# Performance work log

Hardware: AMD Instinct MI355X
Metric: run time of the kernel (lower is better)

Reference implementation:

```python
import jax, jax.numpy as jnp
import numpy as np

CHEB_K = 3


def _cheb(support):
    # Chebyshev polynomial basis [I, A, 2A@T_{k-1} - T_{k-2}] of a dense (N,N) support
    N = support.shape[0]
    ks = [jnp.eye(N, dtype=support.dtype), support]
    for _ in range(2, CHEB_K):
        ks.append(2.0 * support @ ks[-1] - ks[-2])
    return ks


def _agcn(x, sk, W, b):
    # x: (B,N,C); sk: list of (N,N); W: (2*cheb_k*C, O)
    xg = jnp.concatenate([jnp.einsum('nm,bmc->bnc', s, x) for s in sk], axis=-1)
    return jnp.einsum('bni,io->bno', xg, W) + b


def _cell(x, h, sk, Wg, bg, Wu, bu):
    # adaptive graph-conv GRU cell
    hd = h.shape[-1]
    zr = jax.nn.sigmoid(_agcn(jnp.concatenate([x, h], axis=-1), sk, Wg, bg))
    z, r = zr[..., :hd], zr[..., hd:]
    hc = jnp.tanh(_agcn(jnp.concatenate([x, z * h], axis=-1), sk, Wu, bu))
    return r * h + (1.0 - r) * hc


def _forward(x, targets_time, Memory, Wq, We1, We2, egW, egb, euW, eub, dgW, dgb, duW, dub, pW, pb):
    x = jnp.swapaxes(x, 1, -1)  # (B,L,N,C)
    B, L, N, C = x.shape
    H = targets_time.shape[-1]
    ycov = jnp.swapaxes(targets_time, 1, -1)           # (B,H,1,ycov_dim)
    ycov = jnp.broadcast_to(ycov, (B, H, N, ycov.shape[-1]))
    # adaptive adjacency from memory
    e1 = We1 @ Memory
    e2 = We2 @ Memory
    g1 = jax.nn.softmax(jax.nn.relu(e1 @ e2.T), axis=-1)
    g2 = jax.nn.softmax(jax.nn.relu(e2 @ e1.T), axis=-1)
    sk = _cheb(g1) + _cheb(g2)                         # 2*cheb_k supports
    rnn_units = egb.shape[0] // 2
    h0 = jnp.zeros((B, N, rnn_units), x.dtype)
    # encoder: unroll over L (num_layers = 1)
    def enc_step(h, xt):
        return _cell(xt, h, sk, egW, egb, euW, eub), None
    h_t, _ = jax.lax.scan(enc_step, h0, jnp.swapaxes(x, 0, 1))
    # memory attention
    query = h_t @ Wq                                    # (B,N,mem_dim)
    att = jax.nn.softmax(query @ Memory.T, axis=-1)     # (B,N,mem_num)
    h_att = att @ Memory
    h_de = jnp.concatenate([h_t, h_att], axis=-1)       # (B,N,rnn+mem)
    out_dim = pb.shape[0]
    go0 = jnp.zeros((B, N, out_dim), x.dtype)
    def dec_step(carry, yc):
        go, h = carry
        h = _cell(jnp.concatenate([go, yc], axis=-1), h, sk, dgW, dgb, duW, dub)
        go = h @ pW + pb
        return (go, h), go
    _, outs = jax.lax.scan(dec_step, (go0, h_de), jnp.swapaxes(ycov, 0, 1))
    out = jnp.swapaxes(outs, 0, 1)                      # (B,H,N,out_dim)
    return jnp.swapaxes(out, 1, -1)                     # (B,out_dim,N,H)


def setup_inputs() -> dict:
    key = jax.random.key(0)
    ks = jax.random.split(key, 20)
    B, N, L, H = 64, 512, 12, 12
    in_dim, out_dim, ycov_dim = 1, 1, 5
    rnn, mem_num, mem_dim = 64, 20, 64
    dec_dim = rnn + mem_dim
    s = 0.1
    inp = {
        'x': jax.random.normal(ks[0], (B, in_dim, N, L), jnp.float32),
        'adj': jax.random.uniform(ks[1], (N, N), jnp.float32),
        'targets': jax.random.normal(ks[2], (B, out_dim, N, H), jnp.float32),
        'targets_time': jax.random.normal(ks[3], (B, ycov_dim, 1, H), jnp.float32),
        'index': 100,
        'Memory': jax.random.normal(ks[4], (mem_num, mem_dim), jnp.float32) * s,
        'Wq': jax.random.normal(ks[5], (rnn, mem_dim), jnp.float32) * s,
        'We1': jax.random.normal(ks[6], (N, mem_num), jnp.float32) * s,
        'We2': jax.random.normal(ks[7], (N, mem_num), jnp.float32) * s,
        'enc_gate_W': jax.random.normal(ks[8], (2 * CHEB_K * (in_dim + rnn), 2 * rnn), jnp.float32) * s,
        'enc_gate_b': jnp.zeros((2 * rnn,), jnp.float32),
        'enc_upd_W': jax.random.normal(ks[9], (2 * CHEB_K * (in_dim + rnn), rnn), jnp.float32) * s,
        'enc_upd_b': jnp.zeros((rnn,), jnp.float32),
        'dec_gate_W': jax.random.normal(ks[10], (2 * CHEB_K * (out_dim + ycov_dim + dec_dim), 2 * dec_dim), jnp.float32) * s,
        'dec_gate_b': jnp.zeros((2 * dec_dim,), jnp.float32),
        'dec_upd_W': jax.random.normal(ks[11], (2 * CHEB_K * (out_dim + ycov_dim + dec_dim), dec_dim), jnp.float32) * s,
        'dec_upd_b': jnp.zeros((dec_dim,), jnp.float32),
        'proj_W': jax.random.normal(ks[12], (dec_dim, out_dim), jnp.float32) * s,
        'proj_b': jnp.zeros((out_dim,), jnp.float32),
    }
    return inp


def reference(x, adj, targets, targets_time, index, Memory, Wq, We1, We2, enc_gate_W, enc_gate_b, enc_upd_W, enc_upd_b, dec_gate_W, dec_gate_b, dec_upd_W, dec_upd_b, proj_W, proj_b):
    # adj, targets, index only used in training mode; eval path ignores them
    return _forward(x, targets_time, Memory, Wq, We1, We2, enc_gate_W, enc_gate_b, enc_upd_W, enc_upd_b, dec_gate_W, dec_gate_b, dec_upd_W, dec_upd_b, proj_W, proj_b)
```

## Files before the change

### kernel.cpp

```cpp
#include <hip/hip_runtime.h>
#include <hip/hip_bf16.h>
#include <math.h>

typedef __hip_bfloat16 bf16;
typedef __attribute__((ext_vector_type(8))) short s8v;
typedef __attribute__((ext_vector_type(4))) short s4v;
typedef __attribute__((ext_vector_type(4))) float f4v;

#define B_   64
#define N_   512
#define L_   12
#define H_   12
#define RNN  64
#define MEMN 20
#define MEMD 64
#define DD   128
#define NB   32768


__device__ inline void glds16(const bf16* g, bf16* l) {
  __builtin_amdgcn_global_load_lds((const __attribute__((address_space(1))) void*)g,
                                   (__attribute__((address_space(3))) void*)l, 16, 0, 0);
}

__device__ inline int2 xcd_swz() {
  int lid = blockIdx.x + blockIdx.y * gridDim.x;
  int chunk = (gridDim.x * gridDim.y) >> 3;
  int swz = (lid & 7) * chunk + (lid >> 3);
  int bx = swz / gridDim.y;
  int by = swz - bx * gridDim.y;
  return make_int2(bx, by);
}

template<int C_CH, int CP>
__global__ __launch_bounds__(256) void gemm_mix(
    const bf16* __restrict__ Sb, const bf16* __restrict__ XT, bf16* __restrict__ Yb) {
  const int NCOLS = 64 * C_CH;
  __shared__ bf16 As[128 * 32];
  __shared__ bf16 Bs[128 * 32];
  const int tid = threadIdx.x, lane = tid & 63, wid = tid >> 6;
  const int wr = wid >> 1, wc = wid & 1;
  int2 sz = xcd_swz();
  const int bn = sz.x * 128, bm = sz.y * 128;
  const int r_in = lane >> 2, dslot = lane & 3;
  f4v acc[4][4] = {};
  for (int k0 = 0; k0 < 512; k0 += 32) {
#pragma unroll
    for (int h = 0; h < 2; h++) {
      int ci = wid + h * 4;
      int row = ci * 16 + r_in;
      int ss = dslot ^ ((row >> 1) & 3);
      glds16(Sb + (size_t)(bm + row) * 512 + k0 + ss * 8, As + ci * 512);
      glds16(XT + (size_t)(bn + row) * 512 + k0 + ss * 8, Bs + ci * 512);
    }
    asm volatile("s_waitcnt vmcnt(0)" ::: "memory");
    __syncthreads();
    s8v a[4], bb[4];
#pragma unroll
    for (int m = 0; m < 4; m++) {
      int row = wr * 64 + m * 16 + (lane & 15);
      int slot = (lane >> 4) ^ ((row >> 1) & 3);
      a[m] = *(const s8v*)(As + row * 32 + slot * 8);
    }
#pragma unroll
    for (int n = 0; n < 4; n++) {
      int col = wc * 64 + n * 16 + (lane & 15);
      int slot = (lane >> 4) ^ ((col >> 1) & 3);
      bb[n] = *(const s8v*)(Bs + col * 32 + slot * 8);
    }
#pragma unroll
    for (int m = 0; m < 4; m++)
#pragma unroll
      for (int n = 0; n < 4; n++)
        acc[m][n] = __builtin_amdgcn_mfma_f32_16x16x32_bf16(a[m], bb[n], acc[m][n], 0, 0, 0);
    __syncthreads();
  }
#pragma unroll
  for (int m = 0; m < 4; m++) {
#pragma unroll
    for (int rg = 0; rg < 4; rg++) {
      int row = bm + wr * 64 + m * 16 + (lane >> 4) * 4 + rg;
      int s = row >> 9, nn = row & 511;
      size_t obase = (size_t)s * NB * CP;
#pragma unroll
      for (int n = 0; n < 4; n++) {
        int col = bn + wc * 64 + n * 16 + (lane & 15);
        if (col < NCOLS) {
          int b2 = col / C_CH, c = col - b2 * C_CH;
          Yb[obase + (size_t)(b2 * 512 + nn) * CP + c] = __float2bfloat16(acc[m][n][rg]);
        }
      }
    }
  }
}

template<int CP, int EPI, int CCH>
__global__ __launch_bounds__(256) void gemm_proj(
    const bf16* __restrict__ WT, const bf16* __restrict__ XCin,
    const bf16* __restrict__ Yb, const float* __restrict__ bias,
    bf16* __restrict__ RG, float* __restrict__ HT, int hd,
    const float* __restrict__ pW, const float* __restrict__ pb,
    float* __restrict__ outp, bf16* __restrict__ XTo, bf16* __restrict__ XCo,
    bf16* __restrict__ XTa, bf16* __restrict__ XCa, int t) {
  __shared__ bf16 As[128 * 32];
  __shared__ bf16 Bs[64 * 32];
  __shared__ float red2[8 * 64];
  __shared__ float pws[128];
  const int tid = threadIdx.x, lane = tid & 63, wid = tid >> 6;
  const int wr = wid >> 1, wc = wid & 1;
  int2 sz = xcd_swz();
  const int r0 = sz.x * 64, bm = sz.y * 128;
  const int Opad = gridDim.y * 128;
  const int r_in = lane >> 2, dslot = lane & 3;

  if (EPI == 2 && tid < 128) pws[tid] = pW[tid];

  f4v acc[4][2] = {};
#pragma unroll
  for (int seg = 0; seg < 5; seg++) {
    const bf16* Bbase = (seg == 0) ? XCin : (Yb + (size_t)(seg - 1) * NB * CP);
    const bf16* Abase = WT + (size_t)seg * Opad * CP;
    for (int k0 = 0; k0 < CP; k0 += 32) {
#pragma unroll
      for (int h = 0; h < 2; h++) {
        int ci = wid + h * 4;
        int row = ci * 16 + r_in;
        int ss = dslot ^ ((row >> 1) & 3);
        glds16(Abase + (size_t)(bm + row) * CP + k0 + ss * 8, As + ci * 512);
      }
      {
        int row = wid * 16 + r_in;
        int ss = dslot ^ ((row >> 1) & 3);
        glds16(Bbase + (size_t)(r0 + row) * CP + k0 + ss * 8, Bs + wid * 512);
      }
      asm volatile("s_waitcnt vmcnt(0)" ::: "memory");
      __syncthreads();
      s8v a[4], bb[2];
#pragma unroll
      for (int m = 0; m < 4; m++) {
        int row = wr * 64 + m * 16 + (lane & 15);
        int slot = (lane >> 4) ^ ((row >> 1) & 3);
        a[m] = *(const s8v*)(As + row * 32 + slot * 8);
      }
#pragma unroll
      for (int n = 0; n < 2; n++) {
        int col = wc * 32 + n * 16 + (lane & 15);
        int slot = (lane >> 4) ^ ((col >> 1) & 3);
        bb[n] = *(const s8v*)(Bs + col * 32 + slot * 8);
      }
#pragma unroll
      for (int m = 0; m < 4; m++)
#pragma unroll
        for (int n = 0; n < 2; n++)
          acc[m][n] = __builtin_amdgcn_mfma_f32_16x16x32_bf16(a[m], bb[n], acc[m][n], 0, 0, 0);
      __syncthreads();
    }
  }

#pragma unroll
  for (int m = 0; m < 4; m++) {
#pragma unroll
    for (int n = 0; n < 2; n++) {
      int r = r0 + wc * 32 + n * 16 + (lane & 15);
      int b = r >> 9, nn = r & 511;
      int ch0 = bm + wr * 64 + m * 16 + (lane >> 4) * 4;
      if (EPI == 0) {
        if (ch0 < hd) {
          bf16 z4[4];
#pragma unroll
          for (int rg = 0; rg < 4; rg++) {
            int o = ch0 + rg;
            float sg = 1.f / (1.f + expf(-(acc[m][n][rg] + bias[o])));
            float hold = HT[(size_t)o * NB + r];
            z4[rg] = __float2bfloat16(sg * hold);
            XTo[((size_t)b * CCH + o) * 512 + nn] = z4[rg];
          }
          *(s4v*)(XCo + (size_t)r * CP + ch0) = *(const s4v*)z4;
        } else {
#pragma unroll
          for (int rg = 0; rg < 4; rg++) {
            int o = ch0 + rg;
            float sg = 1.f / (1.f + expf(-(acc[m][n][rg] + bias[o])));
            RG[(size_t)(o - hd) * NB + r] = __float2bfloat16(sg);
          }
        }
      } else {
        if (ch0 < hd) {
          bf16 h4[4];
#pragma unroll
          for (int rg = 0; rg < 4; rg++) {
            int o = ch0 + rg;
            float hc = tanhf(acc[m][n][rg] + bias[o]);
            float rgt = __bfloat162float(RG[(size_t)o * NB + r]);
            float* hp = HT + (size_t)o * NB + r;
            float hn = rgt * (*hp) + (1.f - rgt) * hc;
            *hp = hn;
            h4[rg] = __float2bfloat16(hn);
            XTo[((size_t)b * CCH + o) * 512 + nn] = h4[rg];
            acc[m][n][rg] = hn;
          }
          *(s4v*)(XCo + (size_t)r * CP + ch0) = *(const s4v*)h4;
        }
      }
    }
  }

  if (EPI == 2) {
    int slot = wr * 4 + (lane >> 4);
#pragma unroll
    for (int n = 0; n < 2; n++) {
      int r_local = wc * 32 + n * 16 + (lane & 15);
      float ps = 0.f;
#pragma unroll
      for (int m = 0; m < 4; m++)
#pragma unroll
        for (int rg = 0; rg < 4; rg++) {
          int o = wr * 64 + m * 16 + (lane >> 4) * 4 + rg;
          ps += acc[m][n][rg] * pws[o];
        }
      red2[slot * 64 + r_local] = ps;
    }
    __syncthreads();
    if (tid < 64) {
      float v = pb[0];
#pragma unroll
      for (int s2 = 0; s2 < 8; s2++) v += red2[s2 * 64 + tid];
      int r = r0 + tid;
      int b = r >> 9, nn = r & 511;
      outp[b * 6144 + nn * 12 + t] = v;
      bf16 gb = __float2bfloat16(v);
      XTo[((size_t)b * CCH + hd) * 512 + nn] = gb;
      XCo[(size_t)r * CP + hd] = gb;
      XTa[((size_t)b * CCH + hd) * 512 + nn] = gb;
      XCa[(size_t)r * CP + hd] = gb;
    }
  }
}

__global__ __launch_bounds__(256) void gemm_cheb(
    const bf16* __restrict__ A, const bf16* __restrict__ BT, bf16* __restrict__ O) {
  __shared__ bf16 As[128 * 32];
  __shared__ bf16 Bs[128 * 32];
  const int tid = threadIdx.x, lane = tid & 63, wid = tid >> 6;
  const int wr = wid >> 1, wc = wid & 1;
  const int bm = blockIdx.y * 128, bn = blockIdx.x * 128;
  const int r_in = lane >> 2, dslot = lane & 3;
  f4v acc[4][4] = {};
  for (int k0 = 0; k0 < 512; k0 += 32) {
#pragma unroll
    for (int h = 0; h < 2; h++) {
      int ci = wid + h * 4;
      int row = ci * 16 + r_in;
      int ss = dslot ^ ((row >> 1) & 3);
      glds16(A + (size_t)(bm + row) * 512 + k0 + ss * 8, As + ci * 512);
      glds16(BT + (size_t)(bn + row) * 512 + k0 + ss * 8, Bs + ci * 512);
    }
    asm volatile("s_waitcnt vmcnt(0)" ::: "memory");
    __syncthreads();
    s8v a[4], bb[4];
#pragma unroll
    for (int m = 0; m < 4; m++) {
      int row = wr * 64 + m * 16 + (lane & 15);
      int slot = (lane >> 4) ^ ((row >> 1) & 3);
      a[m] = *(const s8v*)(As + row * 32 + slot * 8);
    }
#pragma unroll
    for (int n = 0; n < 4; n++) {
      int col = wc * 64 + n * 16 + (lane & 15);
      int slot = (lane >> 4) ^ ((col >> 1) & 3);
      bb[n] = *(const s8v*)(Bs + col * 32 + slot * 8);
    }
#pragma unroll
    for (int m = 0; m < 4; m++)
#pragma unroll
      for (int n = 0; n < 4; n++)
        acc[m][n] = __builtin_amdgcn_mfma_f32_16x16x32_bf16(a[m], bb[n], acc[m][n], 0, 0, 0);
    __syncthreads();
  }
#pragma unroll
  for (int m = 0; m < 4; m++) {
#pragma unroll
    for (int rg = 0; rg < 4; rg++) {
      int row = bm + wr * 64 + m * 16 + (lane >> 4) * 4 + rg;
#pragma unroll
      for (int n = 0; n < 4; n++) {
        int col = bn + wc * 64 + n * 16 + (lane & 15);
        float v = 2.f * acc[m][n][rg] - (row == col ? 1.f : 0.f);
        O[(size_t)row * 512 + col] = __float2bfloat16(v);
      }
    }
  }
}

__global__ void fill_zero4(float4* p, int n) {
  for (int i = blockIdx.x * 256 + threadIdx.x; i < n; i += gridDim.x * 256)
    p[i] = make_float4(0.f, 0.f, 0.f, 0.f);
}

__global__ void compute_e(const float* __restrict__ We1, const float* __restrict__ We2,
                          const float* __restrict__ Mem, float* __restrict__ e1,
                          float* __restrict__ e2) {
  int idx = blockIdx.x * 256 + threadIdx.x;
  if (idx >= N_ * MEMD) return;
  int n = idx >> 6, d = idx & 63;
  float s1 = 0.f, s2 = 0.f;
  for (int k = 0; k < MEMN; k++) {
    float m = Mem[k * MEMD + d];
    s1 += We1[n * MEMN + k] * m;
    s2 += We2[n * MEMN + k] * m;
  }
  e1[idx] = s1; e2[idx] = s2;
}

__global__ void compute_wqm(const float* __restrict__ Wq, const float* __restrict__ Mem,
                            float* __restrict__ WqM) {
  int idx = blockIdx.x * 256 + threadIdx.x;
  if (idx >= RNN * MEMN) return;
  int c = idx / MEMN, j = idx - c * MEMN;
  float s = 0.f;
  for (int d = 0; d < MEMD; d++) s += Wq[c * MEMD + d] * Mem[j * MEMD + d];
  WqM[idx] = s;
}

__global__ void scores_relu(const float* __restrict__ e1, const float* __restrict__ e2,
                            float* __restrict__ S) {
  int idx = blockIdx.x * 256 + threadIdx.x;
  if (idx >= N_ * N_) return;
  int n = idx >> 9, m = idx & 511;
  float s = 0.f;
  for (int k = 0; k < MEMD; k++) s += e1[n * MEMD + k] * e2[m * MEMD + k];
  S[idx] = s > 0.f ? s : 0.f;
}

__global__ __launch_bounds__(256)
void row_softmax(const float* __restrict__ S, float* __restrict__ G) {
  int r = blockIdx.x;
  __shared__ float red[256];
  float m = -1e30f;
  for (int j = threadIdx.x; j < N_; j += 256) m = fmaxf(m, S[r * N_ + j]);
  red[threadIdx.x] = m; __syncthreads();
  for (int s = 128; s > 0; s >>= 1) {
    if (threadIdx.x < s) red[threadIdx.x] = fmaxf(red[threadIdx.x], red[threadIdx.x + s]);
    __syncthreads();
  }
  m = red[0]; __syncthreads();
  float sum = 0.f;
  for (int j = threadIdx.x; j < N_; j += 256) sum += expf(S[r * N_ + j] - m);
  red[threadIdx.x] = sum; __syncthreads();
  for (int s = 128; s > 0; s >>= 1) {
    if (threadIdx.x < s) red[threadIdx.x] += red[threadIdx.x + s];
    __syncthreads();
  }
  float inv = 1.f / red[0];
  for (int j = threadIdx.x; j < N_; j += 256)
    G[r * N_ + j] = expf(S[r * N_ + j] - m) * inv;
}

__global__ void trans_f32(const float* __restrict__ in, float* __restrict__ outT) {
  __shared__ float t[32][33];
  int bx = blockIdx.x * 32, by = blockIdx.y * 32;
  int x = threadIdx.x, y = threadIdx.y;
  for (int i = 0; i < 32; i += 8) t[y + i][x] = in[(by + y + i) * 512 + bx + x];
  __syncthreads();
  for (int i = 0; i < 32; i += 8) outT[(bx + y + i) * 512 + by + x] = t[x][y + i];
}

__global__ void trans_to_bf16(const float* __restrict__ in, bf16* __restrict__ outN,
                              bf16* __restrict__ outT) {
  __shared__ float t[32][33];
  int bx = blockIdx.x * 32, by = blockIdx.y * 32;
  int x = threadIdx.x, y = threadIdx.y;
  for (int i = 0; i < 32; i += 8) {
    float v = in[(by + y + i) * 512 + bx + x];
    t[y + i][x] = v;
    outN[(by + y + i) * 512 + bx + x] = __float2bfloat16(v);
  }
  __syncthreads();
  for (int i = 0; i < 32; i += 8)
    outT[(bx + y + i) * 512 + by + x] = __float2bfloat16(t[x][y + i]);
}

__global__ void prep_wt(const float* __restrict__ W, bf16* __restrict__ WT,
                        int C, int O, int Opad, int CP, int HD, int MC) {
  int idx = blockIdx.x * 256 + threadIdx.x;
  int tot = 5 * Opad * CP;
  if (idx >= tot) return;
  int seg = idx / (Opad * CP);
  int rem = idx - seg * (Opad * CP);
  int o = rem / CP, c = rem - (rem / CP) * CP;
  float v = 0.f;
  int srcc = -1;
  if (c < HD) srcc = MC + c;
  else if (c < HD + MC) srcc = c - HD;
  if (srcc >= 0 && o < O) {
    const int blkmap[5] = {0, 1, 2, 4, 5};
    int blk = blkmap[seg];
    v = W[(blk * C + srcc) * O + o];
    if (seg == 0) v += W[(3 * C + srcc) * O + o];
  }
  WT[idx] = __float2bfloat16(v);
}

__global__ void fill_misc_enc(bf16* __restrict__ XTh, bf16* __restrict__ XTz,
                              bf16* __restrict__ XCh, bf16* __restrict__ XCz,
                              const float* __restrict__ x, int t) {
  int r = blockIdx.x * 256 + threadIdx.x;
  if (r >= NB) return;
  int b = r >> 9, n = r & 511;
  bf16 v = __float2bfloat16(x[b * 6144 + n * 12 + t]);
  XTh[((size_t)b * 65 + 64) * 512 + n] = v;
  XTz[((size_t)b * 65 + 64) * 512 + n] = v;
  XCh[(size_t)r * 96 + 64] = v;
  XCz[(size_t)r * 96 + 64] = v;
}

__global__ void fill_misc_dec(bf16* __restrict__ XTh, bf16* __restrict__ XTz,
                              bf16* __restrict__ XCh, bf16* __restrict__ XCz,
                              const float* __restrict__ tt, int t, int writego) {
  int idx = blockIdx.x * 256 + threadIdx.x;
  if (idx >= NB * 6) return;
  int ch = idx >> 15, r = idx & (NB - 1);
  int b = r >> 9, n = r & 511;
  bf16 v;
  int c;
  if (ch < 5) { v = __float2bfloat16(tt[b * 60 + ch * 12 + t]); c = 129 + ch; }
  else { if (!writego) return; v = __float2bfloat16(0.f); c = 128; }
  XTh[((size_t)b * 134 + c) * 512 + n] = v;
  XTz[((size_t)b * 134 + c) * 512 + n] = v;
  XCh[(size_t)r * 160 + c] = v;
  XCz[(size_t)r * 160 + c] = v;
}

__global__ __launch_bounds__(128) void attention2(
    const float* __restrict__ HbT, const float* __restrict__ WqM,
    const float* __restrict__ Mem, float* __restrict__ HdT,
    bf16* __restrict__ XTh, bf16* __restrict__ XCh) {
  __shared__ float h[64][128];
  __shared__ float wqm[64][20];
  __shared__ float mem[20][64];
  const int tid = threadIdx.x, r0 = blockIdx.x * 128;
  const int r = r0 + tid, b = r >> 9, n = r & 511;
  for (int e = tid; e < 64 * 128; e += 128) {
    int c = e >> 7, j = e & 127;
    h[c][j] = HbT[(size_t)c * NB + r0 + j];
  }
  for (int e = tid; e < 1280; e += 128) {
    wqm[e / 20][e % 20] = WqM[e];
    mem[e >> 6][e & 63] = Mem[e];
  }
  __syncthreads();
  float s[20];
#pragma unroll
  for (int j = 0; j < 20; j++) s[j] = 0.f;
  for (int c = 0; c < 64; c++) {
    float hv = h[c][tid];
#pragma unroll
    for (int j = 0; j < 20; j++) s[j] += hv * wqm[c][j];
  }
  float mx = s[0];
#pragma unroll
  for (int j = 1; j < 20; j++) mx = fmaxf(mx, s[j]);
  float sum = 0.f;
#pragma unroll
  for (int j = 0; j < 20; j++) { s[j] = expf(s[j] - mx); sum += s[j]; }
  float inv = 1.f / sum;
#pragma unroll
  for (int j = 0; j < 20; j++) s[j] *= inv;
  for (int d = 0; d < 64; d++) {
    float ha = 0.f;
#pragma unroll
    for (int j = 0; j < 20; j++) ha += s[j] * mem[j][d];
    float hv = h[d][tid];
    HdT[(size_t)d * NB + r] = hv;
    HdT[(size_t)(64 + d) * NB + r] = ha;
    bf16 hb = __float2bfloat16(hv), ab = __float2bfloat16(ha);
    XTh[((size_t)b * 134 + d) * 512 + n] = hb;
    XTh[((size_t)b * 134 + 64 + d) * 512 + n] = ab;
    XCh[(size_t)r * 160 + d] = hb;
    XCh[(size_t)r * 160 + 64 + d] = ab;
  }
}

extern "C" void kernel_launch(void* const* d_in, const int* in_sizes, int n_in,
                              void* d_out, int out_size, void* d_ws, size_t ws_size,
                              hipStream_t stream) {
  const float* x   = (const float*)d_in[0];
  const float* tt  = (const float*)d_in[3];
  const float* Mem = (const float*)d_in[5];
  const float* Wq  = (const float*)d_in[6];
  const float* We1 = (const float*)d_in[7];
  const float* We2 = (const float*)d_in[8];
  const float* egW = (const float*)d_in[9];
  const float* egb = (const float*)d_in[10];
  const float* euW = (const float*)d_in[11];
  const float* eub = (const float*)d_in[12];
  const float* dgW = (const float*)d_in[13];
  const float* dgb = (const float*)d_in[14];
  const float* duW = (const float*)d_in[15];
  const float* dub = (const float*)d_in[16];
  const float* pW  = (const float*)d_in[17];
  const float* pb  = (const float*)d_in[18];
  float* out = (float*)d_out;

  char* ws = (char*)d_ws;
  size_t off = 0;
  auto alloc = [&](size_t bytes) { char* p = ws + off; off += (bytes + 255) & ~(size_t)255; return p; };
  bf16* XTh   = (bf16*)alloc((size_t)8576 * 512 * 2);
  bf16* XCh   = (bf16*)alloc((size_t)NB * 160 * 2);
  float* HbT  = (float*)alloc((size_t)RNN * NB * 4);
  size_t zero_bytes = off;
  bf16* XTz   = (bf16*)alloc((size_t)8576 * 512 * 2);
  bf16* XCz   = (bf16*)alloc((size_t)NB * 160 * 2);
  bf16* Ybuf  = (bf16*)alloc((size_t)4 * NB * 160 * 2);
  bf16* RG    = (bf16*)alloc((size_t)DD * NB * 2);
  bf16* WTeg  = (bf16*)alloc((size_t)5 * 128 * 96 * 2);
  bf16* WTeu  = (bf16*)alloc((size_t)5 * 128 * 96 * 2);
  bf16* WTdg  = (bf16*)alloc((size_t)5 * 256 * 160 * 2);
  bf16* WTdu  = (bf16*)alloc((size_t)5 * 128 * 160 * 2);
  bf16* Sb    = (bf16*)alloc((size_t)4 * 512 * 512 * 2);
  bf16* g1T   = (bf16*)alloc((size_t)512 * 512 * 2);
  bf16* g2T   = (bf16*)alloc((size_t)512 * 512 * 2);
  float* HdT  = (float*)alloc((size_t)DD * NB * 4);
  float* WqM  = (float*)alloc((size_t)RNN * MEMN * 4);
  float* e1   = (float*)alloc((size_t)N_ * MEMD * 4);
  float* e2   = (float*)alloc((size_t)N_ * MEMD * 4);
  float* S    = (float*)alloc((size_t)N_ * N_ * 4);
  float* ST   = (float*)alloc((size_t)N_ * N_ * 4);
  float* g1f  = (float*)alloc((size_t)N_ * N_ * 4);
  float* g2f  = (float*)alloc((size_t)N_ * N_ * 4);

  auto blk = [](long n) { return dim3((unsigned)((n + 255) / 256)); };

  fill_zero4<<<2048, 256, 0, stream>>>((float4*)ws, (int)(zero_bytes / 16));
  compute_e<<<blk(N_ * MEMD), 256, 0, stream>>>(We1, We2, Mem, e1, e2);
  compute_wqm<<<blk(RNN * MEMN), 256, 0, stream>>>(Wq, Mem, WqM);
  scores_relu<<<blk(N_ * N_), 256, 0, stream>>>(e1, e2, S);
  trans_f32<<<dim3(16, 16), dim3(32, 8), 0, stream>>>(S, ST);
  row_softmax<<<N_, 256, 0, stream>>>(S, g1f);
  row_softmax<<<N_, 256, 0, stream>>>(ST, g2f);
  trans_to_bf16<<<dim3(16, 16), dim3(32, 8), 0, stream>>>(g1f, Sb + 0 * 262144, g1T);
  trans_to_bf16<<<dim3(16, 16), dim3(32, 8), 0, stream>>>(g2f, Sb + 2 * 262144, g2T);
  gemm_cheb<<<dim3(4, 4), 256, 0, stream>>>(Sb + 0 * 262144, g1T, Sb + 1 * 262144);
  gemm_cheb<<<dim3(4, 4), 256, 0, stream>>>(Sb + 2 * 262144, g2T, Sb + 3 * 262144);
  prep_wt<<<blk(5 * 128 * 96), 256, 0, stream>>>(egW, WTeg, 65, 128, 128, 96, 64, 1);
  prep_wt<<<blk(5 * 128 * 96), 256, 0, stream>>>(euW, WTeu, 65, 64, 128, 96, 64, 1);
  prep_wt<<<blk(5 * 256 * 160), 256, 0, stream>>>(dgW, WTdg, 134, 256, 256, 160, 128, 6);
  prep_wt<<<blk(5 * 128 * 160), 256, 0, stream>>>(duW, WTdu, 134, 128, 128, 160, 128, 6);

  for (int t = 0; t < L_; t++) {
    fill_misc_enc<<<blk(NB), 256, 0, stream>>>(XTh, XTz, XCh, XCz, x, t);
    gemm_mix<65, 96><<<dim3(33, 16), 256, 0, stream>>>(Sb, XTh, Ybuf);
    gemm_proj<96, 0, 65><<<dim3(512, 1), 256, 0, stream>>>(
        WTeg, XCh, Ybuf, egb, RG, HbT, RNN, nullptr, nullptr, nullptr,
        XTz, XCz, nullptr, nullptr, 0);
    gemm_mix<65, 96><<<dim3(33, 16), 256, 0, stream>>>(Sb, XTz, Ybuf);
    gemm_proj<96, 1, 65><<<dim3(512, 1), 256, 0, stream>>>(
        WTeu, XCz, Ybuf, eub, RG, HbT, RNN, nullptr, nullptr, nullptr,
        XTh, XCh, nullptr, nullptr, 0);
  }

  attention2<<<dim3(256), 128, 0, stream>>>(HbT, WqM, Mem, HdT, XTh, XCh);

  for (int t = 0; t < H_; t++) {
    fill_misc_dec<<<blk((long)NB * 6), 256, 0, stream>>>(XTh, XTz, XCh, XCz, tt, t, t == 0);
    gemm_mix<134, 160><<<dim3(67, 16), 256, 0, stream>>>(Sb, XTh, Ybuf);
    gemm_proj<160, 0, 134><<<dim3(512, 2), 256, 0, stream>>>(
        WTdg, XCh, Ybuf, dgb, RG, HdT, DD, nullptr, nullptr, nullptr,
        XTz, XCz, nullptr, nullptr, 0);
    gemm_mix<134, 160><<<dim3(67, 16), 256, 0, stream>>>(Sb, XTz, Ybuf);
    gemm_proj<160, 2, 134><<<dim3(512, 1), 256, 0, stream>>>(
        WTdu, XCz, Ybuf, dub, RG, HdT, DD, pW, pb, out,
        XTh, XCh, XTz, XCz, t);
  }
}
```

Measured before the change: 2.620 ms.

## Fuse graph-mixing GEMM and weight projection into one GRU kernel per gate

Replaces the separate support-mixing GEMM (S@X written to a global Ybuf) and the projection GEMM with a single kernel. Each 512-thread block owns 64 rows and computes the four support products for them, keeping the mixed result in LDS and projecting it straight through the weights. This removes the large intermediate global round-trip and halves the launches per step. The cost is that each block recomputes S-tile loads per 64-row block, the weight fragments are read directly from global memory with no staging, and the inner GEMMs are small with a barrier on every k-step.

```diff
diff --git a/kernel.cpp b/kernel.cpp
--- a/kernel.cpp
+++ b/kernel.cpp
@@ -23,164 +23,151 @@
                                    (__attribute__((address_space(3))) void*)l, 16, 0, 0);
 }
 
-__device__ inline int2 xcd_swz() {
-  int lid = blockIdx.x + blockIdx.y * gridDim.x;
-  int chunk = (gridDim.x * gridDim.y) >> 3;
-  int swz = (lid & 7) * chunk + (lid >> 3);
-  int bx = swz / gridDim.y;
-  int by = swz - bx * gridDim.y;
-  return make_int2(bx, by);
-}
-
-template<int C_CH, int CP>
-__global__ __launch_bounds__(256) void gemm_mix(
-    const bf16* __restrict__ Sb, const bf16* __restrict__ XT, bf16* __restrict__ Yb) {
-  const int NCOLS = 64 * C_CH;
-  __shared__ bf16 As[128 * 32];
-  __shared__ bf16 Bs[128 * 32];
-  const int tid = threadIdx.x, lane = tid & 63, wid = tid >> 6;
-  const int wr = wid >> 1, wc = wid & 1;
-  int2 sz = xcd_swz();
-  const int bn = sz.x * 128, bm = sz.y * 128;
-  const int r_in = lane >> 2, dslot = lane & 3;
-  f4v acc[4][4] = {};
-  for (int k0 = 0; k0 < 512; k0 += 32) {
-#pragma unroll
-    for (int h = 0; h < 2; h++) {
-      int ci = wid + h * 4;
-      int row = ci * 16 + r_in;
-      int ss = dslot ^ ((row >> 1) & 3);
-      glds16(Sb + (size_t)(bm + row) * 512 + k0 + ss * 8, As + ci * 512);
-      glds16(XT + (size_t)(bn + row) * 512 + k0 + ss * 8, Bs + ci * 512);
-    }
-    asm volatile("s_waitcnt vmcnt(0)" ::: "memory");
-    __syncthreads();
-    s8v a[4], bb[4];
-#pragma unroll
-    for (int m = 0; m < 4; m++) {
-      int row = wr * 64 + m * 16 + (lane & 15);
-      int slot = (lane >> 4) ^ ((row >> 1) & 3);
-      a[m] = *(const s8v*)(As + row * 32 + slot * 8);
-    }
-#pragma unroll
-    for (int n = 0; n < 4; n++) {
-      int col = wc * 64 + n * 16 + (lane & 15);
-      int slot = (lane >> 4) ^ ((col >> 1) & 3);
-      bb[n] = *(const s8v*)(Bs + col * 32 + slot * 8);
-    }
-#pragma unroll
-    for (int m = 0; m < 4; m++)
-#pragma unroll
-      for (int n = 0; n < 4; n++)
-        acc[m][n] = __builtin_amdgcn_mfma_f32_16x16x32_bf16(a[m], bb[n], acc[m][n], 0, 0, 0);
-    __syncthreads();
-  }
-#pragma unroll
-  for (int m = 0; m < 4; m++) {
-#pragma unroll
-    for (int rg = 0; rg < 4; rg++) {
-      int row = bm + wr * 64 + m * 16 + (lane >> 4) * 4 + rg;
-      int s = row >> 9, nn = row & 511;
-      size_t obase = (size_t)s * NB * CP;
-#pragma unroll
-      for (int n = 0; n < 4; n++) {
-        int col = bn + wc * 64 + n * 16 + (lane & 15);
-        if (col < NCOLS) {
-          int b2 = col / C_CH, c = col - b2 * C_CH;
-          Yb[obase + (size_t)(b2 * 512 + nn) * CP + c] = __float2bfloat16(acc[m][n][rg]);
-        }
-      }
-    }
-  }
-}
-
-template<int CP, int EPI, int CCH>
-__global__ __launch_bounds__(256) void gemm_proj(
-    const bf16* __restrict__ WT, const bf16* __restrict__ XCin,
-    const bf16* __restrict__ Yb, const float* __restrict__ bias,
-    bf16* __restrict__ RG, float* __restrict__ HT, int hd,
+__device__ inline s8v fragld(const bf16* __restrict__ P, int R0, int ld, int k0, int lane) {
+  return *(const s8v*)(P + (size_t)(R0 + (lane & 15)) * ld + k0 + (lane >> 4) * 8);
+}
+
+template<int C_CH, int CP, int OPAD, int EPI>
+__global__ __launch_bounds__(512) void gru_fused(
+    const bf16* __restrict__ Sb, const bf16* __restrict__ XTin,
+    const bf16* __restrict__ XCin, const bf16* __restrict__ WT,
+    const float* __restrict__ bias, bf16* __restrict__ RG,
+    float* __restrict__ HT, int hd,
     const float* __restrict__ pW, const float* __restrict__ pb,
     float* __restrict__ outp, bf16* __restrict__ XTo, bf16* __restrict__ XCo,
     bf16* __restrict__ XTa, bf16* __restrict__ XCa, int t) {
-  __shared__ bf16 As[128 * 32];
-  __shared__ bf16 Bs[64 * 32];
-  __shared__ float red2[8 * 64];
+  constexpr int YLD = CP + 8;
+  constexpr int MPW = OPAD / 4;
+  constexpr int MF  = MPW / 16;
+  constexpr int CF  = CP / 32;
+  constexpr int NCH = 4 + CP / 16;
+  __shared__ bf16 A1[64 * 32];
+  __shared__ bf16 B1[CP * 32];
+  __shared__ bf16 BsX[64 * 32];
+  __shared__ bf16 Ylds[64 * YLD];
+  __shared__ float red2[16 * 64];
   __shared__ float pws[128];
   const int tid = threadIdx.x, lane = tid & 63, wid = tid >> 6;
-  const int wr = wid >> 1, wc = wid & 1;
-  int2 sz = xcd_swz();
-  const int r0 = sz.x * 64, bm = sz.y * 128;
-  const int Opad = gridDim.y * 128;
+  const int wo = wid >> 1, wn = wid & 1;
+  const int wr1 = wid >> 1, wc1 = wid & 1;
+  int swb = (blockIdx.x & 7) * (gridDim.x >> 3) + (blockIdx.x >> 3);
+  const int r0 = swb * 64;
+  const int b = r0 >> 9, n0 = r0 & 511;
   const int r_in = lane >> 2, dslot = lane & 3;
 
   if (EPI == 2 && tid < 128) pws[tid] = pW[tid];
 
-  f4v acc[4][2] = {};
-#pragma unroll
-  for (int seg = 0; seg < 5; seg++) {
-    const bf16* Bbase = (seg == 0) ? XCin : (Yb + (size_t)(seg - 1) * NB * CP);
-    const bf16* Abase = WT + (size_t)seg * Opad * CP;
-    for (int k0 = 0; k0 < CP; k0 += 32) {
-#pragma unroll
-      for (int h = 0; h < 2; h++) {
-        int ci = wid + h * 4;
-        int row = ci * 16 + r_in;
-        int ss = dslot ^ ((row >> 1) & 3);
-        glds16(Abase + (size_t)(bm + row) * CP + k0 + ss * 8, As + ci * 512);
-      }
-      {
-        int row = wid * 16 + r_in;
-        int ss = dslot ^ ((row >> 1) & 3);
-        glds16(Bbase + (size_t)(r0 + row) * CP + k0 + ss * 8, Bs + wid * 512);
+  f4v acc2[MF][2] = {};
+
+  for (int k0 = 0; k0 < CP; k0 += 32) {
+    if (wid < 4) {
+      int row = wid * 16 + r_in;
+      int ss = dslot ^ ((row >> 1) & 3);
+      glds16(XCin + (size_t)(r0 + row) * CP + k0 + ss * 8, BsX + wid * 512);
+    }
+    asm volatile("s_waitcnt vmcnt(0)" ::: "memory");
+    __syncthreads();
+    s8v a[MF], bb[2];
+#pragma unroll
+    for (int m = 0; m < MF; m++) a[m] = fragld(WT, wo * MPW + m * 16, CP, k0, lane);
+#pragma unroll
+    for (int n = 0; n < 2; n++) {
+      int rl = wn * 32 + n * 16 + (lane & 15);
+      int slot = (lane >> 4) ^ ((rl >> 1) & 3);
+      bb[n] = *(const s8v*)(BsX + rl * 32 + slot * 8);
+    }
+#pragma unroll
+    for (int m = 0; m < MF; m++)
+#pragma unroll
+      for (int n = 0; n < 2; n++)
+        acc2[m][n] = __builtin_amdgcn_mfma_f32_16x16x32_bf16(a[m], bb[n], acc2[m][n], 0, 0, 0);
+    __syncthreads();
+  }
+
+  for (int s = 0; s < 4; s++) {
+    f4v acc1[CF] = {};
+    const bf16* Sbase = Sb + (size_t)s * 512 * 512;
+    for (int k0 = 0; k0 < 512; k0 += 32) {
+      for (int ci = wid; ci < NCH; ci += 8) {
+        if (ci < 4) {
+          int row = ci * 16 + r_in;
+          int ss = dslot ^ ((row >> 1) & 3);
+          glds16(Sbase + (size_t)(n0 + row) * 512 + k0 + ss * 8, A1 + ci * 512);
+        } else {
+          int crow = (ci - 4) * 16 + r_in;
+          int ss = dslot ^ ((crow >> 1) & 3);
+          glds16(XTin + ((size_t)b * C_CH + crow) * 512 + k0 + ss * 8, B1 + (ci - 4) * 512);
+        }
       }
       asm volatile("s_waitcnt vmcnt(0)" ::: "memory");
       __syncthreads();
-      s8v a[4], bb[2];
-#pragma unroll
-      for (int m = 0; m < 4; m++) {
-        int row = wr * 64 + m * 16 + (lane & 15);
+      s8v a1;
+      {
+        int row = wr1 * 16 + (lane & 15);
         int slot = (lane >> 4) ^ ((row >> 1) & 3);
-        a[m] = *(const s8v*)(As + row * 32 + slot * 8);
-      }
+        a1 = *(const s8v*)(A1 + row * 32 + slot * 8);
+      }
+#pragma unroll
+      for (int f = 0; f < CF; f++) {
+        int col = wc1 * (CP / 2) + f * 16 + (lane & 15);
+        int slot = (lane >> 4) ^ ((col >> 1) & 3);
+        s8v b1 = *(const s8v*)(B1 + col * 32 + slot * 8);
+        acc1[f] = __builtin_amdgcn_mfma_f32_16x16x32_bf16(a1, b1, acc1[f], 0, 0, 0);
+      }
+      __syncthreads();
+    }
+#pragma unroll
+    for (int f = 0; f < CF; f++)
+#pragma unroll
+      for (int rg = 0; rg < 4; rg++) {
+        int row = wr1 * 16 + (lane >> 4) * 4 + rg;
+        int col = wc1 * (CP / 2) + f * 16 + (lane & 15);
+        Ylds[row * YLD + col] = __float2bfloat16(acc1[f][rg]);
+      }
+    __syncthreads();
+    const bf16* Ab = WT + (size_t)(s + 1) * OPAD * CP;
+#pragma unroll
+    for (int k0 = 0; k0 < CP; k0 += 32) {
+      s8v a[MF], bb[2];
+#pragma unroll
+      for (int m = 0; m < MF; m++) a[m] = fragld(Ab, wo * MPW + m * 16, CP, k0, lane);
 #pragma unroll
       for (int n = 0; n < 2; n++) {
-        int col = wc * 32 + n * 16 + (lane & 15);
-        int slot = (lane >> 4) ^ ((col >> 1) & 3);
-        bb[n] = *(const s8v*)(Bs + col * 32 + slot * 8);
-      }
-#pragma unroll
-      for (int m = 0; m < 4; m++)
+        int rl = wn * 32 + n * 16 + (lane & 15);
+        bb[n] = *(const s8v*)(Ylds + rl * YLD + k0 + (lane >> 4) * 8);
+      }
+#pragma unroll
+      for (int m = 0; m < MF; m++)
 #pragma unroll
         for (int n = 0; n < 2; n++)
-          acc[m][n] = __builtin_amdgcn_mfma_f32_16x16x32_bf16(a[m], bb[n], acc[m][n], 0, 0, 0);
-      __syncthreads();
-    }
-  }
-
-#pragma unroll
-  for (int m = 0; m < 4; m++) {
+          acc2[m][n] = __builtin_amdgcn_mfma_f32_16x16x32_bf16(a[m], bb[n], acc2[m][n], 0, 0, 0);
+    }
+  }
+
+#pragma unroll
+  for (int m = 0; m < MF; m++) {
 #pragma unroll
     for (int n = 0; n < 2; n++) {
-      int r = r0 + wc * 32 + n * 16 + (lane & 15);
-      int b = r >> 9, nn = r & 511;
-      int ch0 = bm + wr * 64 + m * 16 + (lane >> 4) * 4;
+      int r = r0 + wn * 32 + n * 16 + (lane & 15);
+      int b2 = r >> 9, nn = r & 511;
+      int ch0 = wo * MPW + m * 16 + (lane >> 4) * 4;
       if (EPI == 0) {
         if (ch0 < hd) {
           bf16 z4[4];
 #pragma unroll
           for (int rg = 0; rg < 4; rg++) {
             int o = ch0 + rg;
-            float sg = 1.f / (1.f + expf(-(acc[m][n][rg] + bias[o])));
+            float sg = 1.f / (1.f + expf(-(acc2[m][n][rg] + bias[o])));
             float hold = HT[(size_t)o * NB + r];
             z4[rg] = __float2bfloat16(sg * hold);
-            XTo[((size_t)b * CCH + o) * 512 + nn] = z4[rg];
+            XTo[((size_t)b2 * C_CH + o) * 512 + nn] = z4[rg];
           }
           *(s4v*)(XCo + (size_t)r * CP + ch0) = *(const s4v*)z4;
         } else {
 #pragma unroll
           for (int rg = 0; rg < 4; rg++) {
             int o = ch0 + rg;
-            float sg = 1.f / (1.f + expf(-(acc[m][n][rg] + bias[o])));
+            float sg = 1.f / (1.f + expf(-(acc2[m][n][rg] + bias[o])));
             RG[(size_t)(o - hd) * NB + r] = __float2bfloat16(sg);
           }
         }
@@ -190,14 +177,14 @@
 #pragma unroll
           for (int rg = 0; rg < 4; rg++) {
             int o = ch0 + rg;
-            float hc = tanhf(acc[m][n][rg] + bias[o]);
+            float hc = tanhf(acc2[m][n][rg] + bias[o]);
             float rgt = __bfloat162float(RG[(size_t)o * NB + r]);
             float* hp = HT + (size_t)o * NB + r;
             float hn = rgt * (*hp) + (1.f - rgt) * hc;
             *hp = hn;
             h4[rg] = __float2bfloat16(hn);
-            XTo[((size_t)b * CCH + o) * 512 + nn] = h4[rg];
-            acc[m][n][rg] = hn;
+            XTo[((size_t)b2 * C_CH + o) * 512 + nn] = h4[rg];
+            acc2[m][n][rg] = hn;
           }
           *(s4v*)(XCo + (size_t)r * CP + ch0) = *(const s4v*)h4;
         }
@@ -206,32 +193,32 @@
   }
 
   if (EPI == 2) {
-    int slot = wr * 4 + (lane >> 4);
+    __syncthreads();
 #pragma unroll
     for (int n = 0; n < 2; n++) {
-      int r_local = wc * 32 + n * 16 + (lane & 15);
+      int r_local = wn * 32 + n * 16 + (lane & 15);
       float ps = 0.f;
 #pragma unroll
-      for (int m = 0; m < 4; m++)
+      for (int m = 0; m < MF; m++)
 #pragma unroll
         for (int rg = 0; rg < 4; rg++) {
-          int o = wr * 64 + m * 16 + (lane >> 4) * 4 + rg;
-          ps += acc[m][n][rg] * pws[o];
+          int o = wo * MPW + m * 16 + (lane >> 4) * 4 + rg;
+          ps += acc2[m][n][rg] * pws[o];
         }
-      red2[slot * 64 + r_local] = ps;
+      red2[(wo * 4 + (lane >> 4)) * 64 + r_local] = ps;
     }
     __syncthreads();
     if (tid < 64) {
       float v = pb[0];
 #pragma unroll
-      for (int s2 = 0; s2 < 8; s2++) v += red2[s2 * 64 + tid];
+      for (int s2 = 0; s2 < 16; s2++) v += red2[s2 * 64 + tid];
       int r = r0 + tid;
-      int b = r >> 9, nn = r & 511;
-      outp[b * 6144 + nn * 12 + t] = v;
+      int b2 = r >> 9, nn = r & 511;
+      outp[b2 * 6144 + nn * 12 + t] = v;
       bf16 gb = __float2bfloat16(v);
-      XTo[((size_t)b * CCH + hd) * 512 + nn] = gb;
+      XTo[((size_t)b2 * C_CH + hd) * 512 + nn] = gb;
       XCo[(size_t)r * CP + hd] = gb;
-      XTa[((size_t)b * CCH + hd) * 512 + nn] = gb;
+      XTa[((size_t)b2 * C_CH + hd) * 512 + nn] = gb;
       XCa[(size_t)r * CP + hd] = gb;
     }
   }
@@ -505,16 +492,15 @@
   char* ws = (char*)d_ws;
   size_t off = 0;
   auto alloc = [&](size_t bytes) { char* p = ws + off; off += (bytes + 255) & ~(size_t)255; return p; };
-  bf16* XTh   = (bf16*)alloc((size_t)8576 * 512 * 2);
+  bf16* XTh   = (bf16*)alloc((size_t)8640 * 512 * 2);
   bf16* XCh   = (bf16*)alloc((size_t)NB * 160 * 2);
   float* HbT  = (float*)alloc((size_t)RNN * NB * 4);
   size_t zero_bytes = off;
-  bf16* XTz   = (bf16*)alloc((size_t)8576 * 512 * 2);
+  bf16* XTz   = (bf16*)alloc((size_t)8640 * 512 * 2);
   bf16* XCz   = (bf16*)alloc((size_t)NB * 160 * 2);
-  bf16* Ybuf  = (bf16*)alloc((size_t)4 * NB * 160 * 2);
   bf16* RG    = (bf16*)alloc((size_t)DD * NB * 2);
   bf16* WTeg  = (bf16*)alloc((size_t)5 * 128 * 96 * 2);
-  bf16* WTeu  = (bf16*)alloc((size_t)5 * 128 * 96 * 2);
+  bf16* WTeu  = (bf16*)alloc((size_t)5 * 64 * 96 * 2);
   bf16* WTdg  = (bf16*)alloc((size_t)5 * 256 * 160 * 2);
   bf16* WTdu  = (bf16*)alloc((size_t)5 * 128 * 160 * 2);
   bf16* Sb    = (bf16*)alloc((size_t)4 * 512 * 512 * 2);
@@ -543,19 +529,17 @@
   gemm_cheb<<<dim3(4, 4), 256, 0, stream>>>(Sb + 0 * 262144, g1T, Sb + 1 * 262144);
   gemm_cheb<<<dim3(4, 4), 256, 0, stream>>>(Sb + 2 * 262144, g2T, Sb + 3 * 262144);
   prep_wt<<<blk(5 * 128 * 96), 256, 0, stream>>>(egW, WTeg, 65, 128, 128, 96, 64, 1);
-  prep_wt<<<blk(5 * 128 * 96), 256, 0, stream>>>(euW, WTeu, 65, 64, 128, 96, 64, 1);
+  prep_wt<<<blk(5 * 64 * 96), 256, 0, stream>>>(euW, WTeu, 65, 64, 64, 96, 64, 1);
   prep_wt<<<blk(5 * 256 * 160), 256, 0, stream>>>(dgW, WTdg, 134, 256, 256, 160, 128, 6);
   prep_wt<<<blk(5 * 128 * 160), 256, 0, stream>>>(duW, WTdu, 134, 128, 128, 160, 128, 6);
 
   for (int t = 0; t < L_; t++) {
     fill_misc_enc<<<blk(NB), 256, 0, stream>>>(XTh, XTz, XCh, XCz, x, t);
-    gemm_mix<65, 96><<<dim3(33, 16), 256, 0, stream>>>(Sb, XTh, Ybuf);
-    gemm_proj<96, 0, 65><<<dim3(512, 1), 256, 0, stream>>>(
-        WTeg, XCh, Ybuf, egb, RG, HbT, RNN, nullptr, nullptr, nullptr,
+    gru_fused<65, 96, 128, 0><<<512, 512, 0, stream>>>(
+        Sb, XTh, XCh, WTeg, egb, RG, HbT, RNN, nullptr, nullptr, nullptr,
         XTz, XCz, nullptr, nullptr, 0);
-    gemm_mix<65, 96><<<dim3(33, 16), 256, 0, stream>>>(Sb, XTz, Ybuf);
-    gemm_proj<96, 1, 65><<<dim3(512, 1), 256, 0, stream>>>(
-        WTeu, XCz, Ybuf, eub, RG, HbT, RNN, nullptr, nullptr, nullptr,
+    gru_fused<65, 96, 64, 1><<<512, 512, 0, stream>>>(
+        Sb, XTz, XCz, WTeu, eub, RG, HbT, RNN, nullptr, nullptr, nullptr,
         XTh, XCh, nullptr, nullptr, 0);
   }
 
@@ -563,13 +547,11 @@
 
   for (int t = 0; t < H_; t++) {
     fill_misc_dec<<<blk((long)NB * 6), 256, 0, stream>>>(XTh, XTz, XCh, XCz, tt, t, t == 0);
-    gemm_mix<134, 160><<<dim3(67, 16), 256, 0, stream>>>(Sb, XTh, Ybuf);
-    gemm_proj<160, 0, 134><<<dim3(512, 2), 256, 0, stream>>>(
-        WTdg, XCh, Ybuf, dgb, RG, HdT, DD, nullptr, nullptr, nullptr,
+    gru_fused<134, 160, 256, 0><<<512, 512, 0, stream>>>(
+        Sb, XTh, XCh, WTdg, dgb, RG, HdT, DD, nullptr, nullptr, nullptr,
         XTz, XCz, nullptr, nullptr, 0);
-    gemm_mix<134, 160><<<dim3(67, 16), 256, 0, stream>>>(Sb, XTz, Ybuf);
-    gemm_proj<160, 2, 134><<<dim3(512, 1), 256, 0, stream>>>(
-        WTdu, XCz, Ybuf, dub, RG, HdT, DD, pW, pb, out,
+    gru_fused<134, 160, 128, 2><<<512, 512, 0, stream>>>(
+        Sb, XTz, XCz, WTdu, dub, RG, HdT, DD, pW, pb, out,
         XTh, XCh, XTz, XCz, t);
   }
 }
```

Measured after the change: 2.978 ms. +13.6%, slower.

## Make gemm_proj tile span full output width per block, sized by OPAD template

Applied to the files above, without the earlier changes.

gemm_proj now takes the padded output width as a template parameter, and each block computes all output channels for 64 rows. Each of the four waves owns an OPAD/4 slice of channels across all 64 rows. This removes the second grid row in the decoder gate projection, so the shared activation tiles are loaded once instead of twice. It also stops the encoder update from computing 64 wasted padded channels, since its weights shrink to 64 rows. The cost is larger accumulator and LDS footprints at OPAD=256, which may lower occupancy.

```diff
diff --git a/kernel.cpp b/kernel.cpp
--- a/kernel.cpp
+++ b/kernel.cpp
@@ -94,7 +94,7 @@
   }
 }
 
-template<int CP, int EPI, int CCH>
+template<int CP, int OPAD, int EPI, int CCH>
 __global__ __launch_bounds__(256) void gemm_proj(
     const bf16* __restrict__ WT, const bf16* __restrict__ XCin,
     const bf16* __restrict__ Yb, const float* __restrict__ bias,
@@ -102,68 +102,66 @@
     const float* __restrict__ pW, const float* __restrict__ pb,
     float* __restrict__ outp, bf16* __restrict__ XTo, bf16* __restrict__ XCo,
     bf16* __restrict__ XTa, bf16* __restrict__ XCa, int t) {
-  __shared__ bf16 As[128 * 32];
+  constexpr int MPW = OPAD / 4;
+  constexpr int MF  = MPW / 16;
+  __shared__ bf16 As[OPAD * 32];
   __shared__ bf16 Bs[64 * 32];
-  __shared__ float red2[8 * 64];
+  __shared__ float red2[16 * 64];
   __shared__ float pws[128];
-  const int tid = threadIdx.x, lane = tid & 63, wid = tid >> 6;
-  const int wr = wid >> 1, wc = wid & 1;
-  int2 sz = xcd_swz();
-  const int r0 = sz.x * 64, bm = sz.y * 128;
-  const int Opad = gridDim.y * 128;
+  const int tid = threadIdx.x, lane = tid & 63, wo = tid >> 6;
+  int swb = (blockIdx.x & 7) * (gridDim.x >> 3) + (blockIdx.x >> 3);
+  const int r0 = swb * 64;
   const int r_in = lane >> 2, dslot = lane & 3;
 
   if (EPI == 2 && tid < 128) pws[tid] = pW[tid];
 
-  f4v acc[4][2] = {};
+  f4v acc[MF][4] = {};
 #pragma unroll
   for (int seg = 0; seg < 5; seg++) {
     const bf16* Bbase = (seg == 0) ? XCin : (Yb + (size_t)(seg - 1) * NB * CP);
-    const bf16* Abase = WT + (size_t)seg * Opad * CP;
+    const bf16* Abase = WT + (size_t)seg * OPAD * CP;
     for (int k0 = 0; k0 < CP; k0 += 32) {
-#pragma unroll
-      for (int h = 0; h < 2; h++) {
-        int ci = wid + h * 4;
+      for (int ci = wo; ci < OPAD / 16; ci += 4) {
         int row = ci * 16 + r_in;
         int ss = dslot ^ ((row >> 1) & 3);
-        glds16(Abase + (size_t)(bm + row) * CP + k0 + ss * 8, As + ci * 512);
+        glds16(Abase + (size_t)row * CP + k0 + ss * 8, As + ci * 512);
       }
       {
-        int row = wid * 16 + r_in;
+        int row = wo * 16 + r_in;
         int ss = dslot ^ ((row >> 1) & 3);
-        glds16(Bbase + (size_t)(r0 + row) * CP + k0 + ss * 8, Bs + wid * 512);
+        glds16(Bbase + (size_t)(r0 + row) * CP + k0 + ss * 8, Bs + wo * 512);
       }
       asm volatile("s_waitcnt vmcnt(0)" ::: "memory");
       __syncthreads();
-      s8v a[4], bb[2];
-#pragma unroll
-      for (int m = 0; m < 4; m++) {
-        int row = wr * 64 + m * 16 + (lane & 15);
+      s8v a[MF], bb[4];
+#pragma unroll
+      for (int m = 0; m < MF; m++) {
+        int row = wo * MPW + m * 16 + (lane & 15);
         int slot = (lane >> 4) ^ ((row >> 1) & 3);
         a[m] = *(const s8v*)(As + row * 32 + slot * 8);
       }
 #pragma unroll
-      for (int n = 0; n < 2; n++) {
-        int col = wc * 32 + n * 16 + (lane & 15);
+      for (int n = 0; n < 4; n++) {
+        int col = n * 16 + (lane & 15);
         int slot = (lane >> 4) ^ ((col >> 1) & 3);
         bb[n] = *(const s8v*)(Bs + col * 32 + slot * 8);
       }
 #pragma unroll
-      for (int m = 0; m < 4; m++)
-#pragma unroll
-        for (int n = 0; n < 2; n++)
+      for (int m = 0; m < MF; m++)
+#pragma unroll
+        for (int n = 0; n < 4; n++)
           acc[m][n] = __builtin_amdgcn_mfma_f32_16x16x32_bf16(a[m], bb[n], acc[m][n], 0, 0, 0);
       __syncthreads();
     }
   }
 
 #pragma unroll
-  for (int m = 0; m < 4; m++) {
-#pragma unroll
-    for (int n = 0; n < 2; n++) {
-      int r = r0 + wc * 32 + n * 16 + (lane & 15);
-      int b = r >> 9, nn = r & 511;
-      int ch0 = bm + wr * 64 + m * 16 + (lane >> 4) * 4;
+  for (int m = 0; m < MF; m++) {
+#pragma unroll
+    for (int n = 0; n < 4; n++) {
+      int r = r0 + n * 16 + (lane & 15);
+      int b2 = r >> 9, nn = r & 511;
+      int ch0 = wo * MPW + m * 16 + (lane >> 4) * 4;
       if (EPI == 0) {
         if (ch0 < hd) {
           bf16 z4[4];
@@ -173,7 +171,7 @@
             float sg = 1.f / (1.f + expf(-(acc[m][n][rg] + bias[o])));
             float hold = HT[(size_t)o * NB + r];
             z4[rg] = __float2bfloat16(sg * hold);
-            XTo[((size_t)b * CCH + o) * 512 + nn] = z4[rg];
+            XTo[((size_t)b2 * CCH + o) * 512 + nn] = z4[rg];
           }
           *(s4v*)(XCo + (size_t)r * CP + ch0) = *(const s4v*)z4;
         } else {
@@ -196,7 +194,7 @@
             float hn = rgt * (*hp) + (1.f - rgt) * hc;
             *hp = hn;
             h4[rg] = __float2bfloat16(hn);
-            XTo[((size_t)b * CCH + o) * 512 + nn] = h4[rg];
+            XTo[((size_t)b2 * CCH + o) * 512 + nn] = h4[rg];
             acc[m][n][rg] = hn;
           }
           *(s4v*)(XCo + (size_t)r * CP + ch0) = *(const s4v*)h4;
@@ -206,32 +204,32 @@
   }
 
   if (EPI == 2) {
-    int slot = wr * 4 + (lane >> 4);
-#pragma unroll
-    for (int n = 0; n < 2; n++) {
-      int r_local = wc * 32 + n * 16 + (lane & 15);
+    __syncthreads();
+#pragma unroll
+    for (int n = 0; n < 4; n++) {
+      int r_local = n * 16 + (lane & 15);
       float ps = 0.f;
 #pragma unroll
-      for (int m = 0; m < 4; m++)
+      for (int m = 0; m < MF; m++)
 #pragma unroll
         for (int rg = 0; rg < 4; rg++) {
-          int o = wr * 64 + m * 16 + (lane >> 4) * 4 + rg;
+          int o = wo * MPW + m * 16 + (lane >> 4) * 4 + rg;
           ps += acc[m][n][rg] * pws[o];
         }
-      red2[slot * 64 + r_local] = ps;
+      red2[(wo * 4 + (lane >> 4)) * 64 + r_local] = ps;
     }
     __syncthreads();
     if (tid < 64) {
       float v = pb[0];
 #pragma unroll
-      for (int s2 = 0; s2 < 8; s2++) v += red2[s2 * 64 + tid];
+      for (int s2 = 0; s2 < 16; s2++) v += red2[s2 * 64 + tid];
       int r = r0 + tid;
-      int b = r >> 9, nn = r & 511;
-      outp[b * 6144 + nn * 12 + t] = v;
+      int b2 = r >> 9, nn = r & 511;
+      outp[b2 * 6144 + nn * 12 + t] = v;
       bf16 gb = __float2bfloat16(v);
-      XTo[((size_t)b * CCH + hd) * 512 + nn] = gb;
+      XTo[((size_t)b2 * CCH + hd) * 512 + nn] = gb;
       XCo[(size_t)r * CP + hd] = gb;
-      XTa[((size_t)b * CCH + hd) * 512 + nn] = gb;
+      XTa[((size_t)b2 * CCH + hd) * 512 + nn] = gb;
       XCa[(size_t)r * CP + hd] = gb;
     }
   }
@@ -514,7 +512,7 @@
   bf16* Ybuf  = (bf16*)alloc((size_t)4 * NB * 160 * 2);
   bf16* RG    = (bf16*)alloc((size_t)DD * NB * 2);
   bf16* WTeg  = (bf16*)alloc((size_t)5 * 128 * 96 * 2);
-  bf16* WTeu  = (bf16*)alloc((size_t)5 * 128 * 96 * 2);
+  bf16* WTeu  = (bf16*)alloc((size_t)5 * 64 * 96 * 2);
   bf16* WTdg  = (bf16*)alloc((size_t)5 * 256 * 160 * 2);
   bf16* WTdu  = (bf16*)alloc((size_t)5 * 128 * 160 * 2);
   bf16* Sb    = (bf16*)alloc((size_t)4 * 512 * 512 * 2);
@@ -543,18 +541,18 @@
   gemm_cheb<<<dim3(4, 4), 256, 0, stream>>>(Sb + 0 * 262144, g1T, Sb + 1 * 262144);
   gemm_cheb<<<dim3(4, 4), 256, 0, stream>>>(Sb + 2 * 262144, g2T, Sb + 3 * 262144);
   prep_wt<<<blk(5 * 128 * 96), 256, 0, stream>>>(egW, WTeg, 65, 128, 128, 96, 64, 1);
-  prep_wt<<<blk(5 * 128 * 96), 256, 0, stream>>>(euW, WTeu, 65, 64, 128, 96, 64, 1);
+  prep_wt<<<blk(5 * 64 * 96), 256, 0, stream>>>(euW, WTeu, 65, 64, 64, 96, 64, 1);
   prep_wt<<<blk(5 * 256 * 160), 256, 0, stream>>>(dgW, WTdg, 134, 256, 256, 160, 128, 6);
   prep_wt<<<blk(5 * 128 * 160), 256, 0, stream>>>(duW, WTdu, 134, 128, 128, 160, 128, 6);
 
   for (int t = 0; t < L_; t++) {
     fill_misc_enc<<<blk(NB), 256, 0, stream>>>(XTh, XTz, XCh, XCz, x, t);
     gemm_mix<65, 96><<<dim3(33, 16), 256, 0, stream>>>(Sb, XTh, Ybuf);
-    gemm_proj<96, 0, 65><<<dim3(512, 1), 256, 0, stream>>>(
+    gemm_proj<96, 128, 0, 65><<<512, 256, 0, stream>>>(
         WTeg, XCh, Ybuf, egb, RG, HbT, RNN, nullptr, nullptr, nullptr,
         XTz, XCz, nullptr, nullptr, 0);
     gemm_mix<65, 96><<<dim3(33, 16), 256, 0, stream>>>(Sb, XTz, Ybuf);
-    gemm_proj<96, 1, 65><<<dim3(512, 1), 256, 0, stream>>>(
+    gemm_proj<96, 64, 1, 65><<<512, 256, 0, stream>>>(
         WTeu, XCz, Ybuf, eub, RG, HbT, RNN, nullptr, nullptr, nullptr,
         XTh, XCh, nullptr, nullptr, 0);
   }
@@ -564,11 +562,11 @@
   for (int t = 0; t < H_; t++) {
     fill_misc_dec<<<blk((long)NB * 6), 256, 0, stream>>>(XTh, XTz, XCh, XCz, tt, t, t == 0);
     gemm_mix<134, 160><<<dim3(67, 16), 256, 0, stream>>>(Sb, XTh, Ybuf);
-    gemm_proj<160, 0, 134><<<dim3(512, 2), 256, 0, stream>>>(
+    gemm_proj<160, 256, 0, 134><<<512, 256, 0, stream>>>(
         WTdg, XCh, Ybuf, dgb, RG, HdT, DD, nullptr, nullptr, nullptr,
         XTz, XCz, nullptr, nullptr, 0);
     gemm_mix<134, 160><<<dim3(67, 16), 256, 0, stream>>>(Sb, XTz, Ybuf);
-    gemm_proj<160, 2, 134><<<dim3(512, 1), 256, 0, stream>>>(
+    gemm_proj<160, 128, 2, 134><<<512, 256, 0, stream>>>(
         WTdu, XCz, Ybuf, dub, RG, HdT, DD, pW, pb, out,
         XTh, XCh, XTz, XCz, t);
   }
```

After: 2.602 ms. Within noise of the previous version (-0.7%).
